# Kernel tuning notes

Hardware: AMD Instinct MI355X
Metric: run time of the kernel (lower is better)

The kernel has to match this reference:

```python
import jax, jax.numpy as jnp
import numpy as np

EPS = 1e-12


def setup_inputs() -> dict:
    key = jax.random.key(0)
    k1, k2 = jax.random.split(key)
    ide_feats = jax.random.normal(k1, (4096, 256), dtype=jnp.float32)
    u_feats = jax.random.normal(k2, (16384, 256), dtype=jnp.float32)
    return {"ide_feats": ide_feats, "u_feats": u_feats}


def reference(ide_feats, u_feats):
    # euclidean_dist: sqrt(sum((x_i - y_j)^2) + eps) -> [N, M]
    # computed via the GEMM expansion to avoid the [N, M, D] intermediate
    x2 = jnp.sum(ide_feats * ide_feats, axis=-1)[:, None]   # [N, 1]
    y2 = jnp.sum(u_feats * u_feats, axis=-1)[None, :]       # [1, M]
    xy = jnp.einsum('nd,md->nm', ide_feats, u_feats)        # [N, M]
    d2 = jnp.maximum(x2 + y2 - 2.0 * xy, 0.0)
    dists = jnp.sqrt(d2 + EPS)                              # [N, M]
    d = jnp.mean(dists, axis=-1)                            # [N]
    # dist_loss: sum_{i,j} sqrt((d_i - d_j)^2 + eps)
    diff = d[:, None] - d[None, :]                          # [N, N]
    loss = jnp.sum(jnp.sqrt(diff * diff + EPS))
    return loss
```

## Files before the change

### kernel.cpp

```cpp
#include <hip/hip_runtime.h>
#include <hip/hip_bf16.h>
#include <cstdint>

#define N_IDE 4096
#define M_U   16384
#define D_DIM 256
#define EPSF  1e-12f
#define INV_M (1.0f / 16384.0f)

#define CGC   512
#define BK    32
#define SB_ELEMS (CGC * BK)

typedef _Float16 f16x8 __attribute__((ext_vector_type(8)));
typedef float    f32x4 __attribute__((ext_vector_type(4)));

__device__ __forceinline__ void gll16(const void* g, void* l) {
  __builtin_amdgcn_global_load_lds(
      (const __attribute__((address_space(1))) void*)(uintptr_t)g,
      (__attribute__((address_space(3))) void*)(uint32_t)(uintptr_t)l,
      16, 0, 0);
}

__device__ __forceinline__ unsigned short f2h_bits(float f) {
  _Float16 h = (_Float16)f;
  return __builtin_bit_cast(unsigned short, h);
}

__global__ __launch_bounds__(256) void k_conv(const float* __restrict__ ide,
                                              const float* __restrict__ u,
                                              unsigned short* __restrict__ Ah,
                                              unsigned short* __restrict__ Bh,
                                              float* __restrict__ x2,
                                              float* __restrict__ y2,
                                              float* __restrict__ out) {
  if (blockIdx.x == 0 && threadIdx.x == 0) out[0] = 0.f;
  int gw = (blockIdx.x * 256 + threadIdx.x) >> 6;
  int l  = threadIdx.x & 63;
  const float4* src;
  ushort4* dst;
  float* nrm;
  if (gw < N_IDE) {
    src = (const float4*)(ide + (size_t)gw * D_DIM);
    dst = (ushort4*)(Ah + (size_t)gw * D_DIM);
    nrm = x2 + gw;
  } else {
    int r = gw - N_IDE;
    src = (const float4*)(u + (size_t)r * D_DIM);
    dst = (ushort4*)(Bh + (size_t)r * D_DIM);
    nrm = y2 + r;
  }
  float4 v = src[l];
  float s = v.x * v.x + v.y * v.y + v.z * v.z + v.w * v.w;
  ushort4 o;
  o.x = f2h_bits(v.x); o.y = f2h_bits(v.y);
  o.z = f2h_bits(v.z); o.w = f2h_bits(v.w);
  dst[l] = o;
#pragma unroll
  for (int m = 1; m <= 32; m <<= 1) s += __shfl_xor(s, m, 64);
  if (l == 0) *nrm = s;
}

__global__ __launch_bounds__(512, 2) void k_gemm(const unsigned short* __restrict__ Ah,
                                                 const unsigned short* __restrict__ Bh,
                                                 const float* __restrict__ x2,
                                                 const float* __restrict__ y2,
                                                 float* __restrict__ partial) {
  __shared__ __align__(16) unsigned short sA[128 * 256];
  __shared__ __align__(16) unsigned short sB[2 * SB_ELEMS];
  __shared__ float rowacc[4][128];

  const int t    = threadIdx.x;
  const int w    = t >> 6;
  const int l    = t & 63;
  const int wm   = w >> 2, wn = w & 3;
  const int lrow = l & 15;
  const int lhi  = l >> 4;
  const int bx   = blockIdx.x;
  const int by   = blockIdx.y;

  rowacc[t >> 7][t & 127] = 0.f;

#pragma unroll
  for (int i = 0; i < 8; ++i) {
    int L = i * 512 + t;
    int row = L >> 5;
    int p = L & 31;
    int c = (p & 24) | ((p & 7) ^ (row & 7));
    gll16(Ah + (size_t)(by * 128 + row) * D_DIM + c * 8,
          sA + (size_t)(i * 512 + w * 64) * 8);
  }

  auto stageB = [&](int s) {
    const int cgi = (s >> 3) * 8 + bx;
    const int kt  = s & 7;
    const unsigned short* src = Bh + (size_t)cgi * CGC * D_DIM + kt * BK;
    unsigned short* dstb = sB + (size_t)(s & 1) * SB_ELEMS;
#pragma unroll
    for (int j = 0; j < 4; ++j) {
      int L = j * 512 + t;
      int row = L >> 2;
      int c = L & 3;
      gll16(src + (size_t)row * D_DIM + c * 8,
            dstb + (size_t)(j * 512 + w * 64) * 8);
    }
  };

  float4 x2v[4];
#pragma unroll
  for (int mi = 0; mi < 4; ++mi)
    x2v[mi] = *(const float4*)&x2[by * 128 + wm * 64 + mi * 16 + lhi * 4];

  stageB(0);
  __syncthreads();

  for (int cg = 0; cg < 4; ++cg) {
    const int cgi = cg * 8 + bx;

    f32x4 acc[4][8];
#pragma unroll
    for (int mi = 0; mi < 4; ++mi)
#pragma unroll
      for (int ni = 0; ni < 8; ++ni)
        acc[mi][ni] = (f32x4){0.f, 0.f, 0.f, 0.f};

    for (int kt = 0; kt < 8; ++kt) {
      const int s = cg * 8 + kt;
      if (s + 1 < 32) stageB(s + 1);

      f16x8 af[4];
#pragma unroll
      for (int mi = 0; mi < 4; ++mi) {
        int arow = wm * 64 + mi * 16 + lrow;
        int lc   = kt * 4 + lhi;
        int pc   = (lc & 24) | ((lc & 7) ^ (lrow & 7));
        af[mi] = *(const f16x8*)(sA + (size_t)arow * 256 + pc * 8);
      }

      const unsigned short* bbuf = sB + (size_t)(s & 1) * SB_ELEMS;
#pragma unroll
      for (int half = 0; half < 2; ++half) {
        f16x8 bf[4];
#pragma unroll
        for (int nj = 0; nj < 4; ++nj) {
          int brow = wn * 128 + (half * 4 + nj) * 16 + lrow;
          bf[nj] = *(const f16x8*)(bbuf + (size_t)brow * BK + lhi * 8);
        }
#pragma unroll
        for (int mi = 0; mi < 4; ++mi)
#pragma unroll
          for (int nj = 0; nj < 4; ++nj)
            acc[mi][half * 4 + nj] =
                __builtin_amdgcn_mfma_f32_16x16x32_f16(af[mi], bf[nj],
                                                       acc[mi][half * 4 + nj], 0, 0, 0);
      }
      __syncthreads();
    }

    float yv[8];
#pragma unroll
    for (int ni = 0; ni < 8; ++ni)
      yv[ni] = y2[cgi * CGC + wn * 128 + ni * 16 + lrow];

#pragma unroll
    for (int mi = 0; mi < 4; ++mi) {
      float xr[4] = {x2v[mi].x, x2v[mi].y, x2v[mi].z, x2v[mi].w};
#pragma unroll
      for (int rr = 0; rr < 4; ++rr) {
        float ssum = 0.f;
#pragma unroll
        for (int ni = 0; ni < 8; ++ni) {
          float d2 = xr[rr] + yv[ni] - 2.0f * acc[mi][ni][rr];
          d2 = fmaxf(d2, 0.0f);
          ssum += __builtin_amdgcn_sqrtf(d2 + EPSF);
        }
        ssum += __shfl_xor(ssum, 1, 64);
        ssum += __shfl_xor(ssum, 2, 64);
        ssum += __shfl_xor(ssum, 4, 64);
        ssum += __shfl_xor(ssum, 8, 64);
        if (lrow == 0)
          rowacc[wn][wm * 64 + mi * 16 + lhi * 4 + rr] += ssum;
      }
    }
  }

  __syncthreads();
  if (t < 128)
    partial[(size_t)bx * N_IDE + by * 128 + t] =
        rowacc[0][t] + rowacc[1][t] + rowacc[2][t] + rowacc[3][t];
}

__global__ __launch_bounds__(256) void k_loss(const float* __restrict__ partial,
                                              float* __restrict__ out) {
  __shared__ float sd[N_IDE];
  __shared__ float wsum[4];
  int t = threadIdx.x;
  for (int k = t; k < N_IDE; k += 256) {
    float s = 0.f;
#pragma unroll
    for (int b = 0; b < 8; ++b) s += partial[(size_t)b * N_IDE + k];
    sd[k] = s;
  }
  __syncthreads();
  int tid = blockIdx.x * 256 + t;
  int i   = tid >> 4;
  int jl  = tid & 15;
  float di = sd[i];
  float s  = 0.f;
  for (int k = 0; k < 256; ++k) {
    float diff = (di - sd[jl + k * 16]) * INV_M;
    s += __builtin_amdgcn_sqrtf(diff * diff + EPSF);
  }
#pragma unroll
  for (int m = 1; m <= 32; m <<= 1) s += __shfl_xor(s, m, 64);
  if ((t & 63) == 0) wsum[t >> 6] = s;
  __syncthreads();
  if (t == 0) atomicAdd(out, wsum[0] + wsum[1] + wsum[2] + wsum[3]);
}

extern "C" void kernel_launch(void* const* d_in, const int* in_sizes, int n_in,
                              void* d_out, int out_size, void* d_ws, size_t ws_size,
                              hipStream_t stream) {
  (void)in_sizes; (void)n_in; (void)out_size; (void)ws_size;
  const float* ide = (const float*)d_in[0];
  const float* u   = (const float*)d_in[1];
  float* out = (float*)d_out;

  char* ws = (char*)d_ws;
  size_t off = 0;
  unsigned short* Ah = (unsigned short*)(ws + off); off += (size_t)N_IDE * D_DIM * 2;
  unsigned short* Bh = (unsigned short*)(ws + off); off += (size_t)M_U  * D_DIM * 2;
  float* x2      = (float*)(ws + off); off += (size_t)N_IDE * 4;
  float* y2      = (float*)(ws + off); off += (size_t)M_U * 4;
  float* partial = (float*)(ws + off); off += (size_t)8 * N_IDE * 4;

  k_conv<<<(N_IDE + M_U) / 4, 256, 0, stream>>>(ide, u, Ah, Bh, x2, y2, out);
  k_gemm<<<dim3(8, 32), 512, 0, stream>>>(Ah, Bh, x2, y2, partial);
  k_loss<<<256, 256, 0, stream>>>(partial, out);
}
```

Measured before the change: 126.6 us.

## Fuse fp16 conversion into GEMM kernel with grid-wide arrival counter

Removes the separate conversion kernel. Each GEMM block now converts a 64-row slice of u to fp16 and computes its norms, writing them to global memory. It then converts its own 128 ide rows directly into swizzled LDS, with the row norms kept in shared memory. A global atomic counter with spin-wait makes sure all B conversions finish before the GEMM reads them. This saves a launch and the round trip for A, but it relies on all 256 blocks being co-resident and adds a memset plus grid-wide waiting.

```diff
diff --git a/kernel.cpp b/kernel.cpp
--- a/kernel.cpp
+++ b/kernel.cpp
@@ -14,6 +14,7 @@
 
 typedef _Float16 f16x8 __attribute__((ext_vector_type(8)));
 typedef float    f32x4 __attribute__((ext_vector_type(4)));
+typedef short    short8 __attribute__((ext_vector_type(8)));
 
 __device__ __forceinline__ void gll16(const void* g, void* l) {
   __builtin_amdgcn_global_load_lds(
@@ -27,48 +28,17 @@
   return __builtin_bit_cast(unsigned short, h);
 }
 
-__global__ __launch_bounds__(256) void k_conv(const float* __restrict__ ide,
-                                              const float* __restrict__ u,
-                                              unsigned short* __restrict__ Ah,
-                                              unsigned short* __restrict__ Bh,
-                                              float* __restrict__ x2,
-                                              float* __restrict__ y2,
-                                              float* __restrict__ out) {
-  if (blockIdx.x == 0 && threadIdx.x == 0) out[0] = 0.f;
-  int gw = (blockIdx.x * 256 + threadIdx.x) >> 6;
-  int l  = threadIdx.x & 63;
-  const float4* src;
-  ushort4* dst;
-  float* nrm;
-  if (gw < N_IDE) {
-    src = (const float4*)(ide + (size_t)gw * D_DIM);
-    dst = (ushort4*)(Ah + (size_t)gw * D_DIM);
-    nrm = x2 + gw;
-  } else {
-    int r = gw - N_IDE;
-    src = (const float4*)(u + (size_t)r * D_DIM);
-    dst = (ushort4*)(Bh + (size_t)r * D_DIM);
-    nrm = y2 + r;
-  }
-  float4 v = src[l];
-  float s = v.x * v.x + v.y * v.y + v.z * v.z + v.w * v.w;
-  ushort4 o;
-  o.x = f2h_bits(v.x); o.y = f2h_bits(v.y);
-  o.z = f2h_bits(v.z); o.w = f2h_bits(v.w);
-  dst[l] = o;
-#pragma unroll
-  for (int m = 1; m <= 32; m <<= 1) s += __shfl_xor(s, m, 64);
-  if (l == 0) *nrm = s;
-}
-
-__global__ __launch_bounds__(512, 2) void k_gemm(const unsigned short* __restrict__ Ah,
-                                                 const unsigned short* __restrict__ Bh,
-                                                 const float* __restrict__ x2,
-                                                 const float* __restrict__ y2,
-                                                 float* __restrict__ partial) {
+__global__ __launch_bounds__(512, 2) void k_main(const float* __restrict__ ide,
+                                                 const float* __restrict__ u,
+                                                 unsigned short* __restrict__ Bh,
+                                                 float* __restrict__ y2,
+                                                 float* __restrict__ partial,
+                                                 unsigned int* __restrict__ cnt,
+                                                 float* __restrict__ out) {
   __shared__ __align__(16) unsigned short sA[128 * 256];
   __shared__ __align__(16) unsigned short sB[2 * SB_ELEMS];
   __shared__ float rowacc[4][128];
+  __shared__ float sX[128];
 
   const int t    = threadIdx.x;
   const int w    = t >> 6;
@@ -78,18 +48,70 @@
   const int lhi  = l >> 4;
   const int bx   = blockIdx.x;
   const int by   = blockIdx.y;
-
+  const int blk  = by * 8 + bx;
+
+  if (blk == 0 && t == 0) out[0] = 0.f;
   rowacc[t >> 7][t & 127] = 0.f;
 
-#pragma unroll
-  for (int i = 0; i < 8; ++i) {
-    int L = i * 512 + t;
-    int row = L >> 5;
-    int p = L & 31;
-    int c = (p & 24) | ((p & 7) ^ (row & 7));
-    gll16(Ah + (size_t)(by * 128 + row) * D_DIM + c * 8,
-          sA + (size_t)(i * 512 + w * 64) * 8);
-  }
+  {
+    const float* srcu = u + (size_t)blk * 64 * D_DIM;
+    unsigned short* dstb = Bh + (size_t)blk * 64 * D_DIM;
+#pragma unroll
+    for (int it = 0; it < 4; ++it) {
+      int c = it * 512 + t;
+      int row = c >> 5;
+      int p = c & 31;
+      const float4* s4 = (const float4*)(srcu + (size_t)row * D_DIM + p * 8);
+      float4 a = s4[0], b = s4[1];
+      float sq = a.x*a.x + a.y*a.y + a.z*a.z + a.w*a.w
+               + b.x*b.x + b.y*b.y + b.z*b.z + b.w*b.w;
+      sq += __shfl_xor(sq, 1, 64);  sq += __shfl_xor(sq, 2, 64);
+      sq += __shfl_xor(sq, 4, 64);  sq += __shfl_xor(sq, 8, 64);
+      sq += __shfl_xor(sq, 16, 64);
+      if ((l & 31) == 0) y2[blk * 64 + row] = sq;
+      short8 o;
+      o[0] = (short)f2h_bits(a.x); o[1] = (short)f2h_bits(a.y);
+      o[2] = (short)f2h_bits(a.z); o[3] = (short)f2h_bits(a.w);
+      o[4] = (short)f2h_bits(b.x); o[5] = (short)f2h_bits(b.y);
+      o[6] = (short)f2h_bits(b.z); o[7] = (short)f2h_bits(b.w);
+      *(short8*)(dstb + (size_t)row * D_DIM + p * 8) = o;
+    }
+  }
+  __threadfence();
+  __syncthreads();
+  if (t == 0)
+    __hip_atomic_fetch_add(cnt, 1u, __ATOMIC_RELEASE, __HIP_MEMORY_SCOPE_AGENT);
+
+  {
+    const float* srca = ide + (size_t)by * 128 * D_DIM;
+#pragma unroll
+    for (int i = 0; i < 8; ++i) {
+      int L = i * 512 + t;
+      int row = L >> 5;
+      int p = L & 31;
+      int c = (p & 24) | ((p & 7) ^ (row & 7));
+      const float4* s4 = (const float4*)(srca + (size_t)row * D_DIM + c * 8);
+      float4 a = s4[0], b = s4[1];
+      float sq = a.x*a.x + a.y*a.y + a.z*a.z + a.w*a.w
+               + b.x*b.x + b.y*b.y + b.z*b.z + b.w*b.w;
+      sq += __shfl_xor(sq, 1, 64);  sq += __shfl_xor(sq, 2, 64);
+      sq += __shfl_xor(sq, 4, 64);  sq += __shfl_xor(sq, 8, 64);
+      sq += __shfl_xor(sq, 16, 64);
+      if ((l & 31) == 0) sX[row] = sq;
+      short8 o;
+      o[0] = (short)f2h_bits(a.x); o[1] = (short)f2h_bits(a.y);
+      o[2] = (short)f2h_bits(a.z); o[3] = (short)f2h_bits(a.w);
+      o[4] = (short)f2h_bits(b.x); o[5] = (short)f2h_bits(b.y);
+      o[6] = (short)f2h_bits(b.z); o[7] = (short)f2h_bits(b.w);
+      *(short8*)(sA + (size_t)L * 8) = o;
+    }
+  }
+
+  if (t == 0) {
+    while (__hip_atomic_load(cnt, __ATOMIC_ACQUIRE, __HIP_MEMORY_SCOPE_AGENT) < 256u)
+      __builtin_amdgcn_s_sleep(8);
+  }
+  __syncthreads();
 
   auto stageB = [&](int s) {
     const int cgi = (s >> 3) * 8 + bx;
@@ -109,7 +131,7 @@
   float4 x2v[4];
 #pragma unroll
   for (int mi = 0; mi < 4; ++mi)
-    x2v[mi] = *(const float4*)&x2[by * 128 + wm * 64 + mi * 16 + lhi * 4];
+    x2v[mi] = *(const float4*)&sX[wm * 64 + mi * 16 + lhi * 4];
 
   stageB(0);
   __syncthreads();
@@ -228,13 +250,12 @@
 
   char* ws = (char*)d_ws;
   size_t off = 0;
-  unsigned short* Ah = (unsigned short*)(ws + off); off += (size_t)N_IDE * D_DIM * 2;
-  unsigned short* Bh = (unsigned short*)(ws + off); off += (size_t)M_U  * D_DIM * 2;
-  float* x2      = (float*)(ws + off); off += (size_t)N_IDE * 4;
+  unsigned short* Bh = (unsigned short*)(ws + off); off += (size_t)M_U * D_DIM * 2;
   float* y2      = (float*)(ws + off); off += (size_t)M_U * 4;
   float* partial = (float*)(ws + off); off += (size_t)8 * N_IDE * 4;
-
-  k_conv<<<(N_IDE + M_U) / 4, 256, 0, stream>>>(ide, u, Ah, Bh, x2, y2, out);
-  k_gemm<<<dim3(8, 32), 512, 0, stream>>>(Ah, Bh, x2, y2, partial);
+  unsigned int* cnt = (unsigned int*)(ws + off); off += 64;
+
+  hipMemsetAsync(cnt, 0, sizeof(unsigned int), stream);
+  k_main<<<dim3(8, 32), 512, 0, stream>>>(ide, u, Bh, y2, partial, cnt, out);
   k_loss<<<256, 256, 0, stream>>>(partial, out);
 }
```

Result: slower. 181.1 us (+43.1%).

## Fuse pairwise loss kernel into GEMM via grid-wide atomic barrier

Applied to the files above, without the earlier changes.

Removes the separate k_loss launch by having every GEMM block signal an agent-scope atomic counter and spin until all 256 blocks finish. Each block then rebuilds the row means in shared memory and computes its slice of the pairwise sqrt loss. This saves one kernel launch and the gap between kernels, but it adds a memset, a spin barrier that assumes all 256 blocks are co-resident, and redundant per-block reduction of the partials.

```diff
diff --git a/kernel.cpp b/kernel.cpp
--- a/kernel.cpp
+++ b/kernel.cpp
@@ -65,7 +65,9 @@
                                                  const unsigned short* __restrict__ Bh,
                                                  const float* __restrict__ x2,
                                                  const float* __restrict__ y2,
-                                                 float* __restrict__ partial) {
+                                                 float* __restrict__ partial,
+                                                 unsigned int* __restrict__ cnt,
+                                                 float* __restrict__ out) {
   __shared__ __align__(16) unsigned short sA[128 * 256];
   __shared__ __align__(16) unsigned short sB[2 * SB_ELEMS];
   __shared__ float rowacc[4][128];
@@ -78,6 +80,7 @@
   const int lhi  = l >> 4;
   const int bx   = blockIdx.x;
   const int by   = blockIdx.y;
+  const int blk  = by * 8 + bx;
 
   rowacc[t >> 7][t & 127] = 0.f;
 
@@ -188,34 +191,45 @@
   if (t < 128)
     partial[(size_t)bx * N_IDE + by * 128 + t] =
         rowacc[0][t] + rowacc[1][t] + rowacc[2][t] + rowacc[3][t];
-}
-
-__global__ __launch_bounds__(256) void k_loss(const float* __restrict__ partial,
-                                              float* __restrict__ out) {
-  __shared__ float sd[N_IDE];
-  __shared__ float wsum[4];
-  int t = threadIdx.x;
-  for (int k = t; k < N_IDE; k += 256) {
+
+  __threadfence();
+  __syncthreads();
+  if (t == 0) {
+    __hip_atomic_fetch_add(cnt, 1u, __ATOMIC_RELEASE, __HIP_MEMORY_SCOPE_AGENT);
+    while (__hip_atomic_load(cnt, __ATOMIC_ACQUIRE, __HIP_MEMORY_SCOPE_AGENT) < 256u)
+      __builtin_amdgcn_s_sleep(4);
+  }
+  __syncthreads();
+
+  float* sd = (float*)sA;
+  for (int k = t; k < N_IDE; k += 512) {
     float s = 0.f;
 #pragma unroll
     for (int b = 0; b < 8; ++b) s += partial[(size_t)b * N_IDE + k];
     sd[k] = s;
   }
   __syncthreads();
-  int tid = blockIdx.x * 256 + t;
-  int i   = tid >> 4;
-  int jl  = tid & 15;
-  float di = sd[i];
-  float s  = 0.f;
-  for (int k = 0; k < 256; ++k) {
-    float diff = (di - sd[jl + k * 16]) * INV_M;
-    s += __builtin_amdgcn_sqrtf(diff * diff + EPSF);
-  }
-#pragma unroll
-  for (int m = 1; m <= 32; m <<= 1) s += __shfl_xor(s, m, 64);
-  if ((t & 63) == 0) wsum[t >> 6] = s;
-  __syncthreads();
-  if (t == 0) atomicAdd(out, wsum[0] + wsum[1] + wsum[2] + wsum[3]);
+  {
+    const int gtid = blk * 512 + t;
+    const int i  = gtid >> 5;
+    const int jl = gtid & 31;
+    const float di = sd[i];
+    float s = 0.f;
+    for (int k = 0; k < 128; ++k) {
+      float diff = (di - sd[jl + k * 32]) * INV_M;
+      s += __builtin_amdgcn_sqrtf(diff * diff + EPSF);
+    }
+#pragma unroll
+    for (int m = 1; m <= 32; m <<= 1) s += __shfl_xor(s, m, 64);
+    if (l == 0) rowacc[0][w] = s;
+    __syncthreads();
+    if (t == 0) {
+      float tot = 0.f;
+#pragma unroll
+      for (int q = 0; q < 8; ++q) tot += rowacc[0][q];
+      atomicAdd(out, tot);
+    }
+  }
 }
 
 extern "C" void kernel_launch(void* const* d_in, const int* in_sizes, int n_in,
@@ -233,8 +247,9 @@
   float* x2      = (float*)(ws + off); off += (size_t)N_IDE * 4;
   float* y2      = (float*)(ws + off); off += (size_t)M_U * 4;
   float* partial = (float*)(ws + off); off += (size_t)8 * N_IDE * 4;
-
+  unsigned int* cnt = (unsigned int*)(ws + off); off += 64;
+
+  hipMemsetAsync(cnt, 0, sizeof(unsigned int), stream);
   k_conv<<<(N_IDE + M_U) / 4, 256, 0, stream>>>(ide, u, Ah, Bh, x2, y2, out);
-  k_gemm<<<dim3(8, 32), 512, 0, stream>>>(Ah, Bh, x2, y2, partial);
-  k_loss<<<256, 256, 0, stream>>>(partial, out);
-}
+  k_gemm<<<dim3(8, 32), 512, 0, stream>>>(Ah, Bh, x2, y2, partial, cnt, out);
+}
```

Measured after the change: 165.9 us. 31.1% more time.
